# Optimization experiments

Measured on AMD Instinct MI355X. Metric: run time of the kernel, lower is better.

## Reference

```python
import jax, jax.numpy as jnp
import numpy as np

B, T, D, H = 32, 4096, 512, 512


def setup_inputs() -> dict:
    key = jax.random.key(0)
    ks = jax.random.split(key, 8)
    s = 1.0 / np.sqrt(D)
    return {
        "hidden_state": jax.random.normal(ks[0], (B, D), jnp.float32),
        "encoder_outputs": jax.random.normal(ks[1], (B, T, D), jnp.float32),
        "W": jax.random.normal(ks[2], (D, H), jnp.float32) * s,
        "U": jax.random.normal(ks[3], (D, H), jnp.float32) * s,
        "V": jax.random.normal(ks[4], (H,), jnp.float32) * s,
        "bias": jnp.zeros((H,), jnp.float32),
        "Wa": jax.random.normal(ks[5], (H, H), jnp.float32) * (1.0 / np.sqrt(H)),
        "ba": jnp.zeros((H,), jnp.float32),
    }


def reference(hidden_state, encoder_outputs, W, U, V, bias, Wa, ba):
    # dens1: [B,1,H] ; dens2: [B,T,H]
    dens1 = jnp.einsum('bd,dh->bh', hidden_state, W)[:, None, :]
    dens2 = jnp.einsum('btd,dh->bth', encoder_outputs, U)
    pre = dens1 + dens2 + bias                       # [B,T,H]
    tanh_ = jnp.tanh(jnp.einsum('bth,hk->btk', pre, Wa) + ba)  # extra Dense(tanh)
    cij = jnp.einsum('bth,h->bt', tanh_, V)          # [B,T]
    alphas = jax.nn.softmax(cij, axis=-1)            # [B,T]
    output = jnp.einsum('btd,bt->bd', encoder_outputs, alphas)  # weighted sum
    return output, alphas
```

## Files before the change

kernel.cpp:

```cpp
#include <hip/hip_runtime.h>
#include <hip/hip_bf16.h>


#define BB 32
#define TT 4096
#define DD 512
#define HH 512
#define BK 64

typedef short s16x8 __attribute__((ext_vector_type(8)));
typedef float f32x4 __attribute__((ext_vector_type(4)));

union FU { float f; unsigned u; };

static __device__ __forceinline__ unsigned pack_bf16_trunc(float a, float b) {
    FU ua, ub; ua.f = a; ub.f = b;
    return (ua.u >> 16) | (ub.u & 0xffff0000u);
}

static __device__ __forceinline__ unsigned short f2bf_rne(float x) {
    FU v; v.f = x;
    unsigned u = v.u;
    u = u + 0x7fffu + ((u >> 16) & 1u);
    return (unsigned short)(u >> 16);
}

static __device__ __forceinline__ float tanh_fast(float x) {
    float e = __expf(2.0f * x);
    return 1.0f - 2.0f * __builtin_amdgcn_rcpf(e + 1.0f);
}

static __device__ __forceinline__ void gload_lds16(const void* g, void* l) {
    __builtin_amdgcn_global_load_lds(
        (const __attribute__((address_space(1))) unsigned int*)g,
        (__attribute__((address_space(3))) unsigned int*)l, 16, 0, 0);
}

__global__ void k_dens1(const float* __restrict__ hs, const float* __restrict__ W,
                        const float* __restrict__ bias, float* __restrict__ g) {
    int bi = blockIdx.x;
    int dc = bi & 3, hb = (bi >> 2) & 1, b = bi >> 3;
    int h = hb * 256 + threadIdx.x;
    float s = (dc == 0) ? bias[h] : 0.0f;
    int d0 = dc * 128;
    #pragma unroll 4
    for (int d = 0; d < 128; ++d)
        s = fmaf(hs[b * DD + d0 + d], W[(size_t)(d0 + d) * HH + h], s);
    atomicAdd(&g[b * HH + h], s);
}

__global__ void k_cvec(const float* __restrict__ g, const float* __restrict__ Wa,
                       const float* __restrict__ ba, float* __restrict__ cvec) {
    int bi = blockIdx.x;
    int hc = bi & 3, kb = (bi >> 2) & 1, b = bi >> 3;
    int k = kb * 256 + threadIdx.x;
    float s = (hc == 0) ? ba[k] : 0.0f;
    int h0 = hc * 128;
    #pragma unroll 4
    for (int h = 0; h < 128; ++h)
        s = fmaf(g[b * HH + h0 + h], Wa[(size_t)(h0 + h) * HH + k], s);
    atomicAdd(&cvec[b * HH + k], s);
}

__global__ void k_uwa(const float* __restrict__ U, const float* __restrict__ Wa,
                      unsigned short* __restrict__ UWaT) {
    int d0 = blockIdx.x * 8;
    int tid = threadIdx.x;
    __shared__ float Us[8][DD];
    #pragma unroll
    for (int i = 0; i < 16; ++i) {
        int idx = i * 256 + tid;
        Us[idx >> 9][idx & 511] = U[(size_t)(d0 + (idx >> 9)) * HH + (idx & 511)];
    }
    __syncthreads();
    float acc[8][2] = {};
    #pragma unroll 2
    for (int h = 0; h < DD; ++h) {
        float w0 = Wa[(size_t)h * HH + tid];
        float w1 = Wa[(size_t)h * HH + 256 + tid];
        #pragma unroll
        for (int dd = 0; dd < 8; ++dd) {
            float u = Us[dd][h];
            acc[dd][0] = fmaf(u, w0, acc[dd][0]);
            acc[dd][1] = fmaf(u, w1, acc[dd][1]);
        }
    }
    #pragma unroll
    for (int dd = 0; dd < 8; ++dd) {
        UWaT[(size_t)tid * DD + d0 + dd] = f2bf_rne(acc[dd][0]);
        UWaT[(size_t)(tid + 256) * DD + d0 + dd] = f2bf_rne(acc[dd][1]);
    }
}

__global__ void __launch_bounds__(512, 2) k_gemm_tanh(
    const float* __restrict__ e, const unsigned short* __restrict__ Bt,
    const float* __restrict__ cvec, const float* __restrict__ V,
    float* __restrict__ cij) {
    int tid = threadIdx.x;
    int m0 = blockIdx.x * 128;
    int lane = tid & 63, w = tid >> 6;
    int wr = w >> 2, wc = w & 3;
    int wm = wr * 64, wn = wc * 128;
    int lcol = lane & 15, q = lane >> 4;
    int rl = lane >> 3, gg = lane & 7;

    __shared__ __align__(16) unsigned short As[128 * BK];
    __shared__ __align__(16) unsigned short Bs[512 * BK];

    f32x4 acc[4][8] = {};

    const float* Abase = e + (size_t)m0 * DD;

    for (int k0 = 0; k0 < DD; k0 += BK) {
        float4 av[4];
        #pragma unroll
        for (int it = 0; it < 4; ++it) {
            int idx = it * 512 + tid;
            int row = idx >> 4, c4 = idx & 15;
            av[it] = *(const float4*)(Abase + (size_t)row * DD + k0 + c4 * 4);
        }
        #pragma unroll
        for (int u = 0; u < 8; ++u) {
            int n0 = w * 64 + u * 8;
            const unsigned short* gp =
                Bt + (size_t)(n0 + rl) * DD + k0 + ((gg ^ rl) << 3);
            gload_lds16(gp, &Bs[n0 * 64]);
        }
        #pragma unroll
        for (int it = 0; it < 4; ++it) {
            int idx = it * 512 + tid;
            int row = idx >> 4, c4 = idx & 15;
            uint2 wv;
            wv.x = pack_bf16_trunc(av[it].x, av[it].y);
            wv.y = pack_bf16_trunc(av[it].z, av[it].w);
            int g = c4 >> 1, half = c4 & 1;
            *(uint2*)&As[(g * 128 + (row ^ g)) * 8 + half * 4] = wv;
        }
        __syncthreads();
        #pragma unroll
        for (int ks = 0; ks < BK; ks += 32) {
            int gk = ks >> 3;
            s16x8 af[4], bfr[8];
            #pragma unroll
            for (int i = 0; i < 4; ++i) {
                int row = wm + i * 16 + lcol, g = gk + q;
                af[i] = *(const s16x8*)&As[(g * 128 + (row ^ g)) * 8];
            }
            #pragma unroll
            for (int j = 0; j < 8; ++j) {
                int col = wn + j * 16 + lcol, g = gk + q;
                bfr[j] = *(const s16x8*)&Bs[col * 64 + ((g ^ (col & 7)) << 3)];
            }
            #pragma unroll
            for (int i = 0; i < 4; ++i)
                #pragma unroll
                for (int j = 0; j < 8; ++j)
                    acc[i][j] = __builtin_amdgcn_mfma_f32_16x16x32_bf16(
                        af[i], bfr[j], acc[i][j], 0, 0, 0);
        }
        __syncthreads();
    }

    int b = m0 >> 12;
    float cvv[8], Vv[8];
    #pragma unroll
    for (int j = 0; j < 8; ++j) {
        int h = wn + j * 16 + lcol;
        cvv[j] = cvec[b * HH + h];
        Vv[j] = V[h];
    }
    #pragma unroll
    for (int i = 0; i < 4; ++i) {
        #pragma unroll
        for (int r = 0; r < 4; ++r) {
            float s = 0.0f;
            #pragma unroll
            for (int j = 0; j < 8; ++j)
                s = fmaf(tanh_fast(acc[i][j][r] + cvv[j]), Vv[j], s);
            s += __shfl_xor(s, 1);
            s += __shfl_xor(s, 2);
            s += __shfl_xor(s, 4);
            s += __shfl_xor(s, 8);
            if (lcol == 0)
                atomicAdd(&cij[m0 + wm + i * 16 + q * 4 + r], s);
        }
    }
}

__global__ void k_softmax(const float* __restrict__ cij, float* __restrict__ alphas) {
    int b = blockIdx.x, tid = threadIdx.x;
    const float* row = cij + (size_t)b * TT;
    __shared__ float red[4];
    float m = -1e30f;
    for (int t = tid; t < TT; t += 256) m = fmaxf(m, row[t]);
    #pragma unroll
    for (int o = 1; o < 64; o <<= 1) m = fmaxf(m, __shfl_xor(m, o));
    if ((tid & 63) == 0) red[tid >> 6] = m;
    __syncthreads();
    m = fmaxf(fmaxf(red[0], red[1]), fmaxf(red[2], red[3]));
    __syncthreads();
    float sum = 0.0f;
    for (int t = tid; t < TT; t += 256) sum += __expf(row[t] - m);
    #pragma unroll
    for (int o = 1; o < 64; o <<= 1) sum += __shfl_xor(sum, o);
    if ((tid & 63) == 0) red[tid >> 6] = sum;
    __syncthreads();
    float inv = 1.0f / (red[0] + red[1] + red[2] + red[3]);
    for (int t = tid; t < TT; t += 256)
        alphas[(size_t)b * TT + t] = __expf(row[t] - m) * inv;
}

__global__ void k_wsum(const float* __restrict__ e, const float* __restrict__ alphas,
                       float* __restrict__ pw) {
    int b = blockIdx.x >> 6;
    int chunk = blockIdx.x & 63;
    int t0 = chunk * 64;
    int tid = threadIdx.x;
    int half = tid >> 7, f4 = tid & 127;
    const float* base = e + (size_t)b * TT * DD;
    const float* al = alphas + (size_t)b * TT;
    f32x4 a0 = {0, 0, 0, 0}, a1 = {0, 0, 0, 0};
    for (int it = 0; it < 16; ++it) {
        int t = t0 + it * 4 + half;
        float w0 = al[t], w1 = al[t + 2];
        f32x4 v0 = *(const f32x4*)(base + (size_t)t * DD + f4 * 4);
        f32x4 v1 = *(const f32x4*)(base + (size_t)(t + 2) * DD + f4 * 4);
        a0 += w0 * v0;
        a1 += w1 * v1;
    }
    a0 += a1;
    __shared__ f32x4 red[128];
    if (half == 1) red[f4] = a0;
    __syncthreads();
    if (half == 0) {
        a0 += red[f4];
        *(f32x4*)&pw[((size_t)(b * 64 + chunk)) * DD + f4 * 4] = a0;
    }
}

__global__ void k_wred(const float* __restrict__ pw, float* __restrict__ out) {
    int b = blockIdx.x, tid = threadIdx.x;
    float2 acc = {0.0f, 0.0f};
    const float* base = pw + (size_t)b * 64 * DD;
    #pragma unroll 4
    for (int c = 0; c < 64; ++c) {
        float2 v = *(const float2*)(base + (size_t)c * DD + tid * 2);
        acc.x += v.x;
        acc.y += v.y;
    }
    *(float2*)&out[b * DD + tid * 2] = acc;
}

extern "C" void kernel_launch(void* const* d_in, const int* in_sizes, int n_in,
                              void* d_out, int out_size, void* d_ws, size_t ws_size,
                              hipStream_t stream) {
    const float* hs   = (const float*)d_in[0];
    const float* e    = (const float*)d_in[1];
    const float* W    = (const float*)d_in[2];
    const float* U    = (const float*)d_in[3];
    const float* V    = (const float*)d_in[4];
    const float* bias = (const float*)d_in[5];
    const float* Wa   = (const float*)d_in[6];
    const float* ba   = (const float*)d_in[7];

    float* out    = (float*)d_out;
    float* alphas = out + BB * DD;

    float*          cij  = (float*)d_ws;
    float*          g    = (float*)((char*)d_ws + 524288);
    float*          cvec = (float*)((char*)d_ws + 589824);
    unsigned short* Bt   = (unsigned short*)((char*)d_ws + 655360);
    float*          pw   = (float*)((char*)d_ws + 1179648);

    hipMemsetAsync(d_ws, 0, 655360, stream);

    k_dens1<<<256, 256, 0, stream>>>(hs, W, bias, g);
    k_cvec<<<256, 256, 0, stream>>>(g, Wa, ba, cvec);
    k_uwa<<<64, 256, 0, stream>>>(U, Wa, Bt);
    k_gemm_tanh<<<1024, 512, 0, stream>>>(e, Bt, cvec, V, cij);
    k_softmax<<<BB, 256, 0, stream>>>(cij, alphas);
    k_wsum<<<BB * 64, 256, 0, stream>>>(e, alphas, pw);
    k_wred<<<BB, 256, 0, stream>>>(pw, out);
}
```

Baseline: 569.3 us.

## Double-buffer GEMM tiles, fuse head matvecs, fold softmax into weighted sum

```diff
diff --git a/kernel.cpp b/kernel.cpp
--- a/kernel.cpp
+++ b/kernel.cpp
@@ -36,30 +36,34 @@
         (__attribute__((address_space(3))) unsigned int*)l, 16, 0, 0);
 }
 
-__global__ void k_dens1(const float* __restrict__ hs, const float* __restrict__ W,
-                        const float* __restrict__ bias, float* __restrict__ g) {
-    int bi = blockIdx.x;
-    int dc = bi & 3, hb = (bi >> 2) & 1, b = bi >> 3;
-    int h = hb * 256 + threadIdx.x;
-    float s = (dc == 0) ? bias[h] : 0.0f;
-    int d0 = dc * 128;
-    #pragma unroll 4
-    for (int d = 0; d < 128; ++d)
-        s = fmaf(hs[b * DD + d0 + d], W[(size_t)(d0 + d) * HH + h], s);
-    atomicAdd(&g[b * HH + h], s);
-}
-
-__global__ void k_cvec(const float* __restrict__ g, const float* __restrict__ Wa,
+__global__ void k_head(const float* __restrict__ hs, const float* __restrict__ W,
+                       const float* __restrict__ bias, const float* __restrict__ Wa,
                        const float* __restrict__ ba, float* __restrict__ cvec) {
-    int bi = blockIdx.x;
-    int hc = bi & 3, kb = (bi >> 2) & 1, b = bi >> 3;
-    int k = kb * 256 + threadIdx.x;
-    float s = (hc == 0) ? ba[k] : 0.0f;
-    int h0 = hc * 128;
-    #pragma unroll 4
-    for (int h = 0; h < 128; ++h)
-        s = fmaf(g[b * HH + h0 + h], Wa[(size_t)(h0 + h) * HH + k], s);
-    atomicAdd(&cvec[b * HH + k], s);
+    int b = blockIdx.x, tid = threadIdx.x;
+    __shared__ float hss[DD];
+    __shared__ float gs[HH];
+    if (tid < 128)
+        ((float4*)hss)[tid] = ((const float4*)(hs + (size_t)b * DD))[tid];
+    __syncthreads();
+    float a0 = bias[tid], a1 = bias[tid + 256];
+    #pragma unroll 8
+    for (int d = 0; d < DD; ++d) {
+        float x = hss[d];
+        a0 = fmaf(x, W[(size_t)d * HH + tid], a0);
+        a1 = fmaf(x, W[(size_t)d * HH + 256 + tid], a1);
+    }
+    gs[tid] = a0;
+    gs[tid + 256] = a1;
+    __syncthreads();
+    float c0 = ba[tid], c1 = ba[tid + 256];
+    #pragma unroll 8
+    for (int h = 0; h < HH; ++h) {
+        float x = gs[h];
+        c0 = fmaf(x, Wa[(size_t)h * HH + tid], c0);
+        c1 = fmaf(x, Wa[(size_t)h * HH + 256 + tid], c1);
+    }
+    cvec[(size_t)b * HH + tid] = c0;
+    cvec[(size_t)b * HH + 256 + tid] = c1;
 }
 
 __global__ void k_uwa(const float* __restrict__ U, const float* __restrict__ Wa,
@@ -104,27 +108,25 @@
     int lcol = lane & 15, q = lane >> 4;
     int rl = lane >> 3, gg = lane & 7;
 
-    __shared__ __align__(16) unsigned short As[128 * BK];
-    __shared__ __align__(16) unsigned short Bs[512 * BK];
+    __shared__ __align__(16) unsigned short As[2][128 * BK];
+    __shared__ __align__(16) unsigned short Bs[2][512 * BK];
 
     f32x4 acc[4][8] = {};
-
     const float* Abase = e + (size_t)m0 * DD;
 
-    for (int k0 = 0; k0 < DD; k0 += BK) {
+    {
         float4 av[4];
         #pragma unroll
         for (int it = 0; it < 4; ++it) {
             int idx = it * 512 + tid;
             int row = idx >> 4, c4 = idx & 15;
-            av[it] = *(const float4*)(Abase + (size_t)row * DD + k0 + c4 * 4);
+            av[it] = *(const float4*)(Abase + (size_t)row * DD + c4 * 4);
         }
         #pragma unroll
         for (int u = 0; u < 8; ++u) {
             int n0 = w * 64 + u * 8;
-            const unsigned short* gp =
-                Bt + (size_t)(n0 + rl) * DD + k0 + ((gg ^ rl) << 3);
-            gload_lds16(gp, &Bs[n0 * 64]);
+            gload_lds16(Bt + (size_t)(n0 + rl) * DD + ((gg ^ rl) << 3),
+                        &Bs[0][n0 * 64]);
         }
         #pragma unroll
         for (int it = 0; it < 4; ++it) {
@@ -134,9 +136,33 @@
             wv.x = pack_bf16_trunc(av[it].x, av[it].y);
             wv.y = pack_bf16_trunc(av[it].z, av[it].w);
             int g = c4 >> 1, half = c4 & 1;
-            *(uint2*)&As[(g * 128 + (row ^ g)) * 8 + half * 4] = wv;
+            *(uint2*)&As[0][(g * 128 + (row ^ g)) * 8 + half * 4] = wv;
         }
         __syncthreads();
+    }
+
+    for (int t = 0; t < 8; ++t) {
+        unsigned short* AsC = As[t & 1];
+        unsigned short* BsC = Bs[t & 1];
+        unsigned short* AsN = As[(t & 1) ^ 1];
+        unsigned short* BsN = Bs[(t & 1) ^ 1];
+        float4 av[4];
+        if (t < 7) {
+            int k1 = (t + 1) * BK;
+            #pragma unroll
+            for (int it = 0; it < 4; ++it) {
+                int idx = it * 512 + tid;
+                int row = idx >> 4, c4 = idx & 15;
+                av[it] = *(const float4*)(Abase + (size_t)row * DD + k1 + c4 * 4);
+            }
+            #pragma unroll
+            for (int u = 0; u < 8; ++u) {
+                int n0 = w * 64 + u * 8;
+                gload_lds16(Bt + (size_t)(n0 + rl) * DD + k1 + ((gg ^ rl) << 3),
+                            &BsN[n0 * 64]);
+            }
+        }
+        __builtin_amdgcn_s_setprio(1);
         #pragma unroll
         for (int ks = 0; ks < BK; ks += 32) {
             int gk = ks >> 3;
@@ -144,12 +170,12 @@
             #pragma unroll
             for (int i = 0; i < 4; ++i) {
                 int row = wm + i * 16 + lcol, g = gk + q;
-                af[i] = *(const s16x8*)&As[(g * 128 + (row ^ g)) * 8];
+                af[i] = *(const s16x8*)&AsC[(g * 128 + (row ^ g)) * 8];
             }
             #pragma unroll
             for (int j = 0; j < 8; ++j) {
                 int col = wn + j * 16 + lcol, g = gk + q;
-                bfr[j] = *(const s16x8*)&Bs[col * 64 + ((g ^ (col & 7)) << 3)];
+                bfr[j] = *(const s16x8*)&BsC[col * 64 + ((g ^ (col & 7)) << 3)];
             }
             #pragma unroll
             for (int i = 0; i < 4; ++i)
@@ -158,6 +184,20 @@
                     acc[i][j] = __builtin_amdgcn_mfma_f32_16x16x32_bf16(
                         af[i], bfr[j], acc[i][j], 0, 0, 0);
         }
+        __builtin_amdgcn_s_setprio(0);
+        __builtin_amdgcn_sched_barrier(0);
+        if (t < 7) {
+            #pragma unroll
+            for (int it = 0; it < 4; ++it) {
+                int idx = it * 512 + tid;
+                int row = idx >> 4, c4 = idx & 15;
+                uint2 wv;
+                wv.x = pack_bf16_trunc(av[it].x, av[it].y);
+                wv.y = pack_bf16_trunc(av[it].z, av[it].w);
+                int g = c4 >> 1, half = c4 & 1;
+                *(uint2*)&AsN[(g * 128 + (row ^ g)) * 8 + half * 4] = wv;
+            }
+        }
         __syncthreads();
     }
 
@@ -169,6 +209,7 @@
         cvv[j] = cvec[b * HH + h];
         Vv[j] = V[h];
     }
+    float* redf = (float*)As;
     #pragma unroll
     for (int i = 0; i < 4; ++i) {
         #pragma unroll
@@ -182,12 +223,18 @@
             s += __shfl_xor(s, 4);
             s += __shfl_xor(s, 8);
             if (lcol == 0)
-                atomicAdd(&cij[m0 + wm + i * 16 + q * 4 + r], s);
-        }
-    }
-}
-
-__global__ void k_softmax(const float* __restrict__ cij, float* __restrict__ alphas) {
+                redf[(wm + i * 16 + q * 4 + r) * 4 + wc] = s;
+        }
+    }
+    __syncthreads();
+    if (tid < 128) {
+        float v = redf[tid * 4] + redf[tid * 4 + 1] +
+                  redf[tid * 4 + 2] + redf[tid * 4 + 3];
+        cij[m0 + tid] = v;
+    }
+}
+
+__global__ void k_smstats(const float* __restrict__ cij, float* __restrict__ smst) {
     int b = blockIdx.x, tid = threadIdx.x;
     const float* row = cij + (size_t)b * TT;
     __shared__ float red[4];
@@ -205,24 +252,31 @@
     for (int o = 1; o < 64; o <<= 1) sum += __shfl_xor(sum, o);
     if ((tid & 63) == 0) red[tid >> 6] = sum;
     __syncthreads();
-    float inv = 1.0f / (red[0] + red[1] + red[2] + red[3]);
-    for (int t = tid; t < TT; t += 256)
-        alphas[(size_t)b * TT + t] = __expf(row[t] - m) * inv;
-}
-
-__global__ void k_wsum(const float* __restrict__ e, const float* __restrict__ alphas,
+    if (tid == 0) {
+        smst[b * 2] = m;
+        smst[b * 2 + 1] = 1.0f / (red[0] + red[1] + red[2] + red[3]);
+    }
+}
+
+__global__ void k_wsum(const float* __restrict__ e, const float* __restrict__ cij,
+                       const float* __restrict__ smst, float* __restrict__ alphas,
                        float* __restrict__ pw) {
-    int b = blockIdx.x >> 6;
-    int chunk = blockIdx.x & 63;
+    int bc = (BB * 64 - 1) - blockIdx.x;
+    int b = bc >> 6;
+    int chunk = bc & 63;
     int t0 = chunk * 64;
     int tid = threadIdx.x;
+    float m = smst[b * 2], inv = smst[b * 2 + 1];
+    const float* crow = cij + (size_t)b * TT;
+    if (tid < 64)
+        alphas[(size_t)b * TT + t0 + tid] = __expf(crow[t0 + tid] - m) * inv;
     int half = tid >> 7, f4 = tid & 127;
     const float* base = e + (size_t)b * TT * DD;
-    const float* al = alphas + (size_t)b * TT;
     f32x4 a0 = {0, 0, 0, 0}, a1 = {0, 0, 0, 0};
     for (int it = 0; it < 16; ++it) {
         int t = t0 + it * 4 + half;
-        float w0 = al[t], w1 = al[t + 2];
+        float w0 = __expf(crow[t] - m) * inv;
+        float w1 = __expf(crow[t + 2] - m) * inv;
         f32x4 v0 = *(const f32x4*)(base + (size_t)t * DD + f4 * 4);
         f32x4 v1 = *(const f32x4*)(base + (size_t)(t + 2) * DD + f4 * 4);
         a0 += w0 * v0;
@@ -267,18 +321,15 @@
     float* alphas = out + BB * DD;
 
     float*          cij  = (float*)d_ws;
-    float*          g    = (float*)((char*)d_ws + 524288);
-    float*          cvec = (float*)((char*)d_ws + 589824);
-    unsigned short* Bt   = (unsigned short*)((char*)d_ws + 655360);
+    float*          cvec = (float*)((char*)d_ws + 524288);
+    float*          smst = (float*)((char*)d_ws + 589824);
+    unsigned short* Bt   = (unsigned short*)((char*)d_ws + 593920);
     float*          pw   = (float*)((char*)d_ws + 1179648);
 
-    hipMemsetAsync(d_ws, 0, 655360, stream);
-
-    k_dens1<<<256, 256, 0, stream>>>(hs, W, bias, g);
-    k_cvec<<<256, 256, 0, stream>>>(g, Wa, ba, cvec);
+    k_head<<<BB, 256, 0, stream>>>(hs, W, bias, Wa, ba, cvec);
     k_uwa<<<64, 256, 0, stream>>>(U, Wa, Bt);
     k_gemm_tanh<<<1024, 512, 0, stream>>>(e, Bt, cvec, V, cij);
-    k_softmax<<<BB, 256, 0, stream>>>(cij, alphas);
-    k_wsum<<<BB * 64, 256, 0, stream>>>(e, alphas, pw);
+    k_smstats<<<BB, 256, 0, stream>>>(cij, smst);
+    k_wsum<<<BB * 64, 256, 0, stream>>>(e, cij, smst, alphas, pw);
     k_wred<<<BB, 256, 0, stream>>>(pw, out);
 }
```

Result: no change. 577.3 us (+1.4%).
